# Optimization experiments

Measured on AMD Instinct MI355X. Metric: run time of the kernel, lower is better.

Reference implementation:

```python
import jax, jax.numpy as jnp
import numpy as np

B, S, H = 4, 2048, 1024

def setup_inputs() -> dict:
    key = jax.random.key(0)
    ks = jax.random.split(key, 4)
    scale = 1.0 / np.sqrt(H)
    x = jax.random.normal(ks[0], (B, S, H), dtype=jnp.float32)
    Wq = jax.random.normal(ks[1], (H, H), dtype=jnp.float32) * scale
    Wk = jax.random.normal(ks[2], (H, H), dtype=jnp.float32) * scale
    Wv = jax.random.normal(ks[3], (H, H), dtype=jnp.float32) * scale
    bq = jnp.zeros((H,), dtype=jnp.float32)
    bk = jnp.zeros((H,), dtype=jnp.float32)
    bv = jnp.zeros((H,), dtype=jnp.float32)
    return {"x": x, "Wq": Wq, "bq": bq, "Wk": Wk, "bk": bk, "Wv": Wv, "bv": bv}

def reference(x, Wq, bq, Wk, bk, Wv, bv):
    # Linear: y = x @ W^T + b (torch nn.Linear convention)
    Q = jnp.einsum('bsh,oh->bso', x, Wq) + bq
    K = jnp.einsum('bsh,oh->bso', x, Wk) + bk
    V = jnp.einsum('bsh,oh->bso', x, Wv) + bv
    scores = jnp.einsum('bqh,bkh->bqk', Q, K) / jnp.sqrt(jnp.float32(H))
    attn = jax.nn.softmax(scores, axis=-1)
    return jnp.einsum('bqk,bkh->bqh', attn, V)
```

## Files before the change

### kernel.cpp

```cpp
#include <hip/hip_runtime.h>
#include <cstdint>
#include <cstddef>


typedef __bf16 bf16;
typedef _Float16 f16;
typedef __bf16 bf16x8 __attribute__((ext_vector_type(8)));
typedef __bf16 bf16x4 __attribute__((ext_vector_type(4)));
typedef float f32x4 __attribute__((ext_vector_type(4)));

#define BM 128
#define BN 128
#define BK 64

__global__ __launch_bounds__(256)
void cvt_f32_bf16(const float* __restrict__ src, bf16* __restrict__ dst, int n4)
{
    const int i = blockIdx.x * 256 + threadIdx.x;
    if (i < n4) {
        f32x4 v = *(const f32x4*)(src + 4 * (size_t)i);
        bf16x4 o;
#pragma unroll
        for (int r = 0; r < 4; ++r) o[r] = (bf16)v[r];
        *(bf16x4*)(dst + 4 * (size_t)i) = o;
    }
}

__device__ __forceinline__ void stage_tile(const bf16* __restrict__ g, int ld,
                                           bf16* lds_generic, int tid)
{
    auto lds3 = (__attribute__((address_space(3))) char*)lds_generic;
    const int wave = tid >> 6;
#pragma unroll
    for (int issue = 0; issue < 4; ++issue) {
        const int p   = issue * 256 + tid;
        const int row = p >> 3;
        const int cp  = p & 7;
        const int c   = cp ^ (row & 7);
        const bf16* gp = g + (size_t)row * ld + c * 8;
        const unsigned wave_base = (unsigned)(issue * 4096 + wave * 1024);
        __builtin_amdgcn_global_load_lds(
            (const __attribute__((address_space(1))) void*)gp,
            (__attribute__((address_space(3))) void*)(lds3 + wave_base),
            16, 0, 0);
    }
}

__device__ __forceinline__ bf16x8 read_frag(const bf16* lds, int row, int chunk)
{
    const int cp = chunk ^ (row & 7);
    return *(const bf16x8*)(lds + row * BK + cp * 8);
}

template <int OUTMODE>
__global__ __launch_bounds__(256)
void gemm_bt(const bf16* __restrict__ A, const bf16* __restrict__ Bm,
             const float* __restrict__ bias0, const float* __restrict__ bias1,
             const float* __restrict__ bias2, void* __restrict__ C,
             int K, int N, float alpha, long zA, long zB, long zC)
{
    __shared__ alignas(16) bf16 As[2][BM * BK];
    __shared__ alignas(16) bf16 Bs[2][BN * BK];

    const int tid  = threadIdx.x;
    const int lane = tid & 63;
    const int wid  = tid >> 6;
    const int wr   = (wid >> 1) * 64;
    const int wc   = (wid & 1) * 64;
    const int quad = lane >> 4;
    const int l16  = lane & 15;

    const int m0 = blockIdx.y * BM;
    const int n0 = blockIdx.x * BN;
    const int z  = blockIdx.z;

    const bf16* Ab = A + (size_t)z * zA + (size_t)m0 * K;
    const bf16* Bb = Bm + (size_t)z * zB + (size_t)n0 * K;

    f32x4 acc[4][4] = {};

    stage_tile(Ab, K, As[0], tid);
    stage_tile(Bb, K, Bs[0], tid);

    const int niter = K / BK;
    for (int it = 0; it < niter; ++it) {
        const int cur = it & 1;
        __syncthreads();
        if (it + 1 < niter) {
            stage_tile(Ab + (it + 1) * BK, K, As[cur ^ 1], tid);
            stage_tile(Bb + (it + 1) * BK, K, Bs[cur ^ 1], tid);
        }
#pragma unroll
        for (int h = 0; h < 2; ++h) {
            bf16x8 af[4], bfr[4];
#pragma unroll
            for (int i = 0; i < 4; ++i)
                af[i]  = read_frag(As[cur], wr + i * 16 + l16, h * 4 + quad);
#pragma unroll
            for (int j = 0; j < 4; ++j)
                bfr[j] = read_frag(Bs[cur], wc + j * 16 + l16, h * 4 + quad);

#pragma unroll
            for (int i = 0; i < 4; ++i)
#pragma unroll
                for (int j = 0; j < 4; ++j)
                    acc[i][j] = __builtin_amdgcn_mfma_f32_16x16x32_bf16(
                        af[i], bfr[j], acc[i][j], 0, 0, 0);
        }
    }

#pragma unroll
    for (int j = 0; j < 4; ++j) {
        const int col3 = n0 + wc + j * 16 + l16;
#pragma unroll
        for (int i = 0; i < 4; ++i) {
            const int rbase = m0 + wr + i * 16 + quad * 4;
            if (OUTMODE == 2) {
                f16* Cf = (f16*)C + (size_t)z * zC;
#pragma unroll
                for (int r = 0; r < 4; ++r)
                    Cf[(size_t)(rbase + r) * N + col3] = (f16)(acc[i][j][r] * alpha);
            } else if (OUTMODE == 3) {
                float* Cf = (float*)C + (size_t)z * zC;
#pragma unroll
                for (int r = 0; r < 4; ++r)
                    Cf[(size_t)(rbase + r) * N + col3] = acc[i][j][r];
            } else {
                const int mat = col3 >> 10;
                const int col = col3 & 1023;
                const float* bp = (mat == 0) ? bias0 : (mat == 1) ? bias1 : bias2;
                const float bj = bp[col];
                if (mat < 2) {
                    bf16* Cb = (bf16*)C + (size_t)mat * (8u << 20);
#pragma unroll
                    for (int r = 0; r < 4; ++r)
                        Cb[(size_t)(rbase + r) * 1024 + col] =
                            (bf16)(acc[i][j][r] + bj);
                } else {
                    bf16* Cb = (bf16*)C + (size_t)(16u << 20);
                    const int b = rbase >> 11;
                    const int s = rbase & 2047;
                    bf16x4 tmp;
#pragma unroll
                    for (int r = 0; r < 4; ++r) tmp[r] = (bf16)(acc[i][j][r] + bj);
                    *(bf16x4*)(Cb + (((size_t)((b << 10) + col)) << 11) + s) = tmp;
                }
            }
        }
    }
}

__device__ __forceinline__ float wred_max(float v)
{
#pragma unroll
    for (int o = 32; o > 0; o >>= 1) v = fmaxf(v, __shfl_xor(v, o, 64));
    return v;
}
__device__ __forceinline__ float wred_sum(float v)
{
#pragma unroll
    for (int o = 32; o > 0; o >>= 1) v += __shfl_xor(v, o, 64);
    return v;
}

__global__ __launch_bounds__(256)
void softmax_rows(const f16* __restrict__ Sc, bf16* __restrict__ P)
{
    constexpr int NC = 2048;
    const size_t row = blockIdx.x;
    const f16* src = Sc + row * NC;
    bf16* dst = P + row * NC;
    const int tid = threadIdx.x;

    float v[8];
    float m = -3.4e38f;
#pragma unroll
    for (int i = 0; i < 8; ++i) {
        v[i] = (float)src[tid + 256 * i];
        m = fmaxf(m, v[i]);
    }
    m = wred_max(m);

    __shared__ float redm[4], reds[4];
    if ((tid & 63) == 0) redm[tid >> 6] = m;
    __syncthreads();
    m = fmaxf(fmaxf(redm[0], redm[1]), fmaxf(redm[2], redm[3]));

    float s = 0.f;
#pragma unroll
    for (int i = 0; i < 8; ++i) { v[i] = __expf(v[i] - m); s += v[i]; }
    s = wred_sum(s);
    if ((tid & 63) == 0) reds[tid >> 6] = s;
    __syncthreads();
    s = reds[0] + reds[1] + reds[2] + reds[3];

    const float inv = 1.f / s;
#pragma unroll
    for (int i = 0; i < 8; ++i) dst[tid + 256 * i] = (bf16)(v[i] * inv);
}

extern "C" void kernel_launch(void* const* d_in, const int* in_sizes, int n_in,
                              void* d_out, int out_size, void* d_ws, size_t ws_size,
                              hipStream_t stream)
{
    constexpr int B = 4, S = 2048, H = 1024;
    const float* x  = (const float*)d_in[0];
    const float* Wq = (const float*)d_in[1];
    const float* bq = (const float*)d_in[2];
    const float* Wk = (const float*)d_in[3];
    const float* bk = (const float*)d_in[4];
    const float* Wv = (const float*)d_in[5];
    const float* bv = (const float*)d_in[6];
    float* out = (float*)d_out;

    char* ws = (char*)d_ws;
    bf16* xb   = (bf16*)ws;
    bf16* Wqkv = (bf16*)(ws + (size_t)(16 << 20));
    bf16* Q    = (bf16*)(ws + (size_t)(22 << 20));
    bf16* Kp   = (bf16*)(ws + (size_t)(38 << 20));
    bf16* Vt   = (bf16*)(ws + (size_t)(54 << 20));
    f16*  Sc   = (f16*) (ws + (size_t)(70 << 20));
    bf16* P    = (bf16*)(ws + (size_t)(22 << 20));

    dim3 blk(256, 1, 1);

    cvt_f32_bf16<<<dim3((B * S * H) / 1024), blk, 0, stream>>>(x, xb, (B * S * H) / 4);
    cvt_f32_bf16<<<dim3((H * H) / 1024), blk, 0, stream>>>(Wq, Wqkv, (H * H) / 4);
    cvt_f32_bf16<<<dim3((H * H) / 1024), blk, 0, stream>>>(Wk, Wqkv + (size_t)H * H, (H * H) / 4);
    cvt_f32_bf16<<<dim3((H * H) / 1024), blk, 0, stream>>>(Wv, Wqkv + 2 * (size_t)H * H, (H * H) / 4);

    gemm_bt<4><<<dim3(3 * H / BN, (B * S) / BM, 1), blk, 0, stream>>>(
        xb, Wqkv, bq, bk, bv, Q, H, 3 * H, 1.0f, 0, 0, 0);

    gemm_bt<2><<<dim3(S / BN, S / BM, B), blk, 0, stream>>>(
        Q, Kp, nullptr, nullptr, nullptr, Sc, H, S, 0.03125f,
        (long)S * H, (long)S * H, (long)S * S);

    softmax_rows<<<dim3(B * S), blk, 0, stream>>>(Sc, P);

    gemm_bt<3><<<dim3(H / BN, S / BM, B), blk, 0, stream>>>(
        P, Vt, nullptr, nullptr, nullptr, out, S, H, 1.0f,
        (long)S * S, (long)H * S, (long)S * H);
}
```

Baseline: 264.1 us.

## Fuse conversion launches and single-buffer LDS in attention GEMMs for occupancy

The four fp32-to-bf16 conversion launches are merged into one kernel that routes each index to x or to one of the three weight matrices. The GEMM gains a template flag that selects double or single LDS buffering. The QK^T and PV GEMMs now use a single buffer with a second barrier per iteration, which halves their LDS footprint and raises the launch-bounds occupancy hint from 2 to 4 blocks. This trades overlap of global loads with MFMA work for more resident waves to hide latency.

```diff
diff --git a/kernel.cpp b/kernel.cpp
--- a/kernel.cpp
+++ b/kernel.cpp
@@ -13,17 +13,32 @@
 #define BN 128
 #define BK 64
 
+#define XQ (8388608 / 4)
+#define WQ (1048576 / 4)
 __global__ __launch_bounds__(256)
-void cvt_f32_bf16(const float* __restrict__ src, bf16* __restrict__ dst, int n4)
+void cvt_all(const float* __restrict__ x, const float* __restrict__ Wq,
+             const float* __restrict__ Wk, const float* __restrict__ Wv,
+             bf16* __restrict__ xb, bf16* __restrict__ Wqkv)
 {
     const int i = blockIdx.x * 256 + threadIdx.x;
-    if (i < n4) {
-        f32x4 v = *(const f32x4*)(src + 4 * (size_t)i);
-        bf16x4 o;
-#pragma unroll
-        for (int r = 0; r < 4; ++r) o[r] = (bf16)v[r];
-        *(bf16x4*)(dst + 4 * (size_t)i) = o;
-    }
+    const float* src;
+    bf16* dst;
+    if (i < XQ) {
+        src = x + 4 * (size_t)i;
+        dst = xb + 4 * (size_t)i;
+    } else {
+        const int j = i - XQ;
+        const int w = j / WQ;
+        const int off = j - w * WQ;
+        const float* ws_ = (w == 0) ? Wq : (w == 1) ? Wk : Wv;
+        src = ws_ + 4 * (size_t)off;
+        dst = Wqkv + 4 * (size_t)j;
+    }
+    f32x4 v = *(const f32x4*)src;
+    bf16x4 o;
+#pragma unroll
+    for (int r = 0; r < 4; ++r) o[r] = (bf16)v[r];
+    *(bf16x4*)dst = o;
 }
 
 __device__ __forceinline__ void stage_tile(const bf16* __restrict__ g, int ld,
@@ -52,15 +67,15 @@
     return *(const bf16x8*)(lds + row * BK + cp * 8);
 }
 
-template <int OUTMODE>
-__global__ __launch_bounds__(256)
+template <int OUTMODE, int DBUF>
+__global__ __launch_bounds__(256, DBUF ? 2 : 4)
 void gemm_bt(const bf16* __restrict__ A, const bf16* __restrict__ Bm,
              const float* __restrict__ bias0, const float* __restrict__ bias1,
              const float* __restrict__ bias2, void* __restrict__ C,
              int K, int N, float alpha, long zA, long zB, long zC)
 {
-    __shared__ alignas(16) bf16 As[2][BM * BK];
-    __shared__ alignas(16) bf16 Bs[2][BN * BK];
+    __shared__ alignas(16) bf16 As[DBUF + 1][BM * BK];
+    __shared__ alignas(16) bf16 Bs[DBUF + 1][BN * BK];
 
     const int tid  = threadIdx.x;
     const int lane = tid & 63;
@@ -79,16 +94,27 @@
 
     f32x4 acc[4][4] = {};
 
-    stage_tile(Ab, K, As[0], tid);
-    stage_tile(Bb, K, Bs[0], tid);
+    if (DBUF) {
+        stage_tile(Ab, K, As[0], tid);
+        stage_tile(Bb, K, Bs[0], tid);
+    }
 
     const int niter = K / BK;
     for (int it = 0; it < niter; ++it) {
-        const int cur = it & 1;
-        __syncthreads();
-        if (it + 1 < niter) {
-            stage_tile(Ab + (it + 1) * BK, K, As[cur ^ 1], tid);
-            stage_tile(Bb + (it + 1) * BK, K, Bs[cur ^ 1], tid);
+        int cur;
+        if (DBUF) {
+            cur = it & 1;
+            __syncthreads();
+            if (it + 1 < niter) {
+                stage_tile(Ab + (it + 1) * BK, K, As[cur ^ 1], tid);
+                stage_tile(Bb + (it + 1) * BK, K, Bs[cur ^ 1], tid);
+            }
+        } else {
+            cur = 0;
+            __syncthreads();
+            stage_tile(Ab + it * BK, K, As[0], tid);
+            stage_tile(Bb + it * BK, K, Bs[0], tid);
+            __syncthreads();
         }
 #pragma unroll
         for (int h = 0; h < 2; ++h) {
@@ -224,21 +250,19 @@
 
     dim3 blk(256, 1, 1);
 
-    cvt_f32_bf16<<<dim3((B * S * H) / 1024), blk, 0, stream>>>(x, xb, (B * S * H) / 4);
-    cvt_f32_bf16<<<dim3((H * H) / 1024), blk, 0, stream>>>(Wq, Wqkv, (H * H) / 4);
-    cvt_f32_bf16<<<dim3((H * H) / 1024), blk, 0, stream>>>(Wk, Wqkv + (size_t)H * H, (H * H) / 4);
-    cvt_f32_bf16<<<dim3((H * H) / 1024), blk, 0, stream>>>(Wv, Wqkv + 2 * (size_t)H * H, (H * H) / 4);
-
-    gemm_bt<4><<<dim3(3 * H / BN, (B * S) / BM, 1), blk, 0, stream>>>(
+    cvt_all<<<dim3((XQ + 3 * WQ) / 256), blk, 0, stream>>>(
+        x, Wq, Wk, Wv, xb, Wqkv);
+
+    gemm_bt<4, 1><<<dim3(3 * H / BN, (B * S) / BM, 1), blk, 0, stream>>>(
         xb, Wqkv, bq, bk, bv, Q, H, 3 * H, 1.0f, 0, 0, 0);
 
-    gemm_bt<2><<<dim3(S / BN, S / BM, B), blk, 0, stream>>>(
+    gemm_bt<2, 0><<<dim3(S / BN, S / BM, B), blk, 0, stream>>>(
         Q, Kp, nullptr, nullptr, nullptr, Sc, H, S, 0.03125f,
         (long)S * H, (long)S * H, (long)S * S);
 
     softmax_rows<<<dim3(B * S), blk, 0, stream>>>(Sc, P);
 
-    gemm_bt<3><<<dim3(H / BN, S / BM, B), blk, 0, stream>>>(
+    gemm_bt<3, 0><<<dim3(H / BN, S / BM, B), blk, 0, stream>>>(
         P, Vt, nullptr, nullptr, nullptr, out, S, H, 1.0f,
         (long)S * S, (long)H * S, (long)S * H);
 }
```

Measured after the change: 264.1 us. About the same (-0.0%).
